# Optimization experiments

Measured on AMD Instinct MI355X. Metric: run time of the kernel, lower is better.

The kernel has to match this reference:

```python
import jax, jax.numpy as jnp
import numpy as np

N = 1 << 20          # number of sample points (rays x samples)
ENC = 32             # hash-grid encoded dim (16 levels x 2 features)
HID = 64
GEO = 15


def setup_inputs() -> dict:
    key = jax.random.key(0)
    ks = jax.random.split(key, 16)
    sc = lambda fan_in: 1.0 / np.sqrt(fan_in)
    return {
        "x": jax.random.normal(ks[0], (N, ENC), jnp.float32),
        "d": jax.random.normal(ks[1], (N, ENC), jnp.float32),
        # sigma net: ENC -> 64 -> 64 -> 1+GEO, bias-free, stored [in, out]
        "Ws0": jax.random.normal(ks[2], (ENC, HID), jnp.float32) * sc(ENC),
        "Ws1": jax.random.normal(ks[3], (HID, HID), jnp.float32) * sc(HID),
        "Ws2": jax.random.normal(ks[4], (HID, 1 + GEO), jnp.float32) * sc(HID),
        # color net: ENC+GEO -> 64 -> 64 -> 64 -> 3, bias-free
        "Wc0": jax.random.normal(ks[5], (ENC + GEO, HID), jnp.float32) * sc(ENC + GEO),
        "Wc1": jax.random.normal(ks[6], (HID, HID), jnp.float32) * sc(HID),
        "Wc2": jax.random.normal(ks[7], (HID, HID), jnp.float32) * sc(HID),
        "Wc3": jax.random.normal(ks[8], (HID, 3), jnp.float32) * sc(HID),
    }


def reference(x, d, Ws0, Ws1, Ws2, Wc0, Wc1, Wc2, Wc3):
    # sigma network: ReLU after EVERY layer (including the last, as in source)
    h = x
    for W in (Ws0, Ws1, Ws2):
        h = jax.nn.relu(h @ W)
    sigma = h[..., 0]            # [N]
    geo_feat = h[..., 1:]        # [N, GEO]

    # color network: ReLU on all but last layer, then sigmoid
    h = jnp.concatenate([d, geo_feat], axis=-1)   # [N, ENC+GEO]
    color_ws = (Wc0, Wc1, Wc2, Wc3)
    for i, W in enumerate(color_ws):
        h = h @ W
        if i != len(color_ws) - 1:
            h = jax.nn.relu(h)
    color = jax.nn.sigmoid(h)    # [N, 3]
    return color, sigma
```

## Files before the change

kernel.cpp:

```cpp
#include <hip/hip_runtime.h>
#include <hip/hip_bf16.h>

typedef short s8v __attribute__((ext_vector_type(8)));
typedef float f4v __attribute__((ext_vector_type(4)));

#define MFMA_BF16 __builtin_amdgcn_mfma_f32_16x16x32_bf16

constexpr int OFF_W0T  = 0;
constexpr int OFF_W1T  = 2560;
constexpr int OFF_W2T  = 7168;
constexpr int OFF_WC0T = 8320;
constexpr int OFF_WC1T = 12928;
constexpr int OFF_WC2T = 17536;
constexpr int OFF_WC3T = 22144;
constexpr int OFF_H    = 23296;
constexpr int SMEM_EL  = OFF_H + 8 * 2048;

static __device__ __forceinline__ short bf2s(__hip_bfloat16 h) {
    union { __hip_bfloat16 b; short s; } u; u.b = h; return u.s;
}

__global__ __launch_bounds__(512, 4)
void rf_fused(const void* __restrict__ xv,
              const void* __restrict__ dv,
              const void* __restrict__ Ws0,
              const void* __restrict__ Ws1,
              const void* __restrict__ Ws2,
              const void* __restrict__ Wc0,
              const void* __restrict__ Wc1,
              const void* __restrict__ Wc2,
              const void* __restrict__ Wc3,
              void* __restrict__ outp,
              int npts)
{
    __shared__ __align__(16) short smem[SMEM_EL];
    __shared__ int cls_cnt;
    const int t = threadIdx.x;

    if (t == 0) cls_cnt = 0;
    __syncthreads();
    {
        unsigned short w = ((const unsigned short*)xv)[2 * t];
        int e = (w >> 7) & 0xFF;
        if (e >= 110 && e <= 140) atomicAdd(&cls_cnt, 1);
    }
    __syncthreads();
    const bool isbf = (cls_cnt >= 256);

    auto ldw = [&](const void* p, int idx) -> short {
        if (isbf) return ((const short*)p)[idx];
        return bf2s(__float2bfloat16(((const float*)p)[idx]));
    };

    for (int i = t; i < 2048; i += 512) { int k = i >> 6, n = i & 63; smem[OFF_W0T  + n*40 + k] = ldw(Ws0, i); }
    for (int i = t; i < 4096; i += 512) { int k = i >> 6, n = i & 63; smem[OFF_W1T  + n*72 + k] = ldw(Ws1, i); }
    for (int i = t; i < 1024; i += 512) { int k = i >> 4, n = i & 15; smem[OFF_W2T  + n*72 + k] = ldw(Ws2, i); }
    for (int i = t; i < 4096; i += 512) { int n = i >> 6, k = i & 63; smem[OFF_WC0T + n*72 + k] = (k < 47) ? ldw(Wc0, k*64 + n) : (short)0; }
    for (int i = t; i < 4096; i += 512) { int k = i >> 6, n = i & 63; smem[OFF_WC1T + n*72 + k] = ldw(Wc1, i); }
    for (int i = t; i < 4096; i += 512) { int k = i >> 6, n = i & 63; smem[OFF_WC2T + n*72 + k] = ldw(Wc2, i); }
    for (int i = t; i < 1024; i += 512) { int n = i >> 6, k = i & 63; smem[OFF_WC3T + n*72 + k] = (n < 3) ? ldw(Wc3, k*3 + n) : (short)0; }
    __syncthreads();

    const int lane = t & 63;
    const int wv   = t >> 6;
    const int m16  = lane & 15;
    const int q    = lane >> 4;
    short* sH = smem + OFF_H + wv * 2048;

    auto hAddr = [&](int row, int col) -> int {
        return row*64 + ((((col >> 3) ^ (row & 7))) << 3) + (col & 7);
    };

    const f4v zf = {0.f, 0.f, 0.f, 0.f};

    auto loadRow8f = [&](const void* p, int eoff) -> s8v {
        const float* f = (const float*)p + eoff;
        f4v f0 = *(const f4v*)f;
        f4v f1 = *(const f4v*)(f + 4);
        s8v r;
        #pragma unroll
        for (int j = 0; j < 4; j++) {
            r[j]     = bf2s(__float2bfloat16(f0[j]));
            r[j + 4] = bf2s(__float2bfloat16(f1[j]));
        }
        return r;
    };
    auto putOut = [&](int idx, float v) {
        if (isbf) ((short*)outp)[idx] = bf2s(__float2bfloat16(v));
        else      ((float*)outp)[idx] = v;
    };

    auto loadAH = [&](s8v (&af)[2][2]) {
        asm volatile("" ::: "memory");
        #pragma unroll
        for (int mt = 0; mt < 2; mt++)
            #pragma unroll
            for (int ks = 0; ks < 2; ks++)
                af[mt][ks] = *(const s8v*)(sH + (mt*16 + m16)*64 + (((ks*4 + q) ^ (m16 & 7)) << 3));
    };
    auto layer64 = [&](int woff, f4v (&a)[2][4], const s8v (&af)[2][2]) {
        #pragma unroll
        for (int nt = 0; nt < 4; nt++) {
            s8v b0 = *(const s8v*)(smem + woff + (nt*16 + m16)*72 + q*8);
            s8v b1 = *(const s8v*)(smem + woff + (nt*16 + m16)*72 + 32 + q*8);
            #pragma unroll
            for (int mt = 0; mt < 2; mt++)
                a[mt][nt] = MFMA_BF16(af[mt][1], b1, MFMA_BF16(af[mt][0], b0, zf, 0,0,0), 0,0,0);
        }
    };
    auto storeH64 = [&](const f4v (&a)[2][4]) {
        #pragma unroll
        for (int mt = 0; mt < 2; mt++)
            #pragma unroll
            for (int nt = 0; nt < 4; nt++)
                #pragma unroll
                for (int r = 0; r < 4; r++) {
                    int row = mt*16 + q*4 + r;
                    sH[row*64 + (((nt*2 + (m16 >> 3)) ^ (row & 7)) << 3) + (m16 & 7)] =
                        bf2s(__float2bfloat16(fmaxf(a[mt][nt][r], 0.f)));
                }
        asm volatile("" ::: "memory");
    };

    const int ntiles = npts / 32;
    const int tstep  = gridDim.x * 8;
    int tile = blockIdx.x * 8 + wv;

    s8v xr[2], dr[2];
    if (isbf && tile < ntiles) {
        #pragma unroll
        for (int mt = 0; mt < 2; mt++) {
            const int off = (tile*32 + mt*16 + m16)*32 + q*8;
            xr[mt] = *(const s8v*)((const short*)xv + off);
            dr[mt] = *(const s8v*)((const short*)dv + off);
        }
    }

    for (; tile < ntiles; tile += tstep) {
        const int r0  = tile * 32;
        const int nxt = tile + tstep;

        s8v xrn[2], drn[2];
        if (isbf && nxt < ntiles) {
            #pragma unroll
            for (int mt = 0; mt < 2; mt++) {
                const int off = (nxt*32 + mt*16 + m16)*32 + q*8;
                xrn[mt] = *(const s8v*)((const short*)xv + off);
                drn[mt] = *(const s8v*)((const short*)dv + off);
            }
        }

        s8v xa[2], da[2];
        if (isbf) {
            xa[0] = xr[0]; xa[1] = xr[1];
            da[0] = dr[0]; da[1] = dr[1];
        } else {
            #pragma unroll
            for (int mt = 0; mt < 2; mt++) {
                const int off = (r0 + mt*16 + m16)*32 + q*8;
                xa[mt] = loadRow8f(xv, off);
                da[mt] = loadRow8f(dv, off);
            }
        }

        f4v acc[2][4];

        #pragma unroll
        for (int nt = 0; nt < 4; nt++) {
            s8v b = *(const s8v*)(smem + OFF_W0T + (nt*16 + m16)*40 + q*8);
            #pragma unroll
            for (int mt = 0; mt < 2; mt++)
                acc[mt][nt] = MFMA_BF16(xa[mt], b, zf, 0,0,0);
        }
        storeH64(acc);

        s8v a2[2][2];
        loadAH(a2);
        layer64(OFF_W1T, acc, a2);
        storeH64(acc);

        s8v a3[2][2];
        loadAH(a3);
        s8v c0 = *(const s8v*)(smem + OFF_W2T + m16*72 + q*8);
        s8v c1 = *(const s8v*)(smem + OFF_W2T + m16*72 + 32 + q*8);
        f4v acc3[2];
        #pragma unroll
        for (int mt = 0; mt < 2; mt++)
            acc3[mt] = MFMA_BF16(a3[mt][1], c1, MFMA_BF16(a3[mt][0], c0, zf, 0,0,0), 0,0,0);

        #pragma unroll
        for (int mt = 0; mt < 2; mt++)
            #pragma unroll
            for (int r = 0; r < 4; r++) {
                float v = fmaxf(acc3[mt][r], 0.f);
                int row = mt*16 + q*4 + r;
                if (m16 == 0) {
                    putOut(3*npts + r0 + row, v);
                    sH[hAddr(row, 15)] = 0;
                } else {
                    sH[hAddr(row, m16 - 1)] = bf2s(__float2bfloat16(v));
                }
            }
        asm volatile("" ::: "memory");

        s8v ga[2];
        #pragma unroll
        for (int mt = 0; mt < 2; mt++)
            ga[mt] = *(const s8v*)(sH + (mt*16 + m16)*64 + ((q ^ (m16 & 7)) << 3));
        #pragma unroll
        for (int nt = 0; nt < 4; nt++) {
            s8v b0 = *(const s8v*)(smem + OFF_WC0T + (nt*16 + m16)*72 + q*8);
            s8v b1 = *(const s8v*)(smem + OFF_WC0T + (nt*16 + m16)*72 + 32 + q*8);
            #pragma unroll
            for (int mt = 0; mt < 2; mt++)
                acc[mt][nt] = MFMA_BF16(ga[mt], b1, MFMA_BF16(da[mt], b0, zf, 0,0,0), 0,0,0);
        }
        storeH64(acc);

        s8v a5[2][2];
        loadAH(a5);
        layer64(OFF_WC1T, acc, a5);
        storeH64(acc);

        s8v a6[2][2];
        loadAH(a6);
        layer64(OFF_WC2T, acc, a6);
        storeH64(acc);

        s8v a7[2][2];
        loadAH(a7);
        s8v e0 = *(const s8v*)(smem + OFF_WC3T + m16*72 + q*8);
        s8v e1 = *(const s8v*)(smem + OFF_WC3T + m16*72 + 32 + q*8);
        f4v acc7[2];
        #pragma unroll
        for (int mt = 0; mt < 2; mt++)
            acc7[mt] = MFMA_BF16(a7[mt][1], e1, MFMA_BF16(a7[mt][0], e0, zf, 0,0,0), 0,0,0);

        if (m16 < 3) {
            #pragma unroll
            for (int mt = 0; mt < 2; mt++)
                #pragma unroll
                for (int r = 0; r < 4; r++) {
                    float v  = acc7[mt][r];
                    float sg = 1.0f / (1.0f + __expf(-v));
                    putOut((r0 + mt*16 + q*4 + r)*3 + m16, sg);
                }
        }

        if (isbf) {
            xr[0] = xrn[0]; xr[1] = xrn[1];
            dr[0] = drn[0]; dr[1] = drn[1];
        }
    }
}

extern "C" void kernel_launch(void* const* d_in, const int* in_sizes, int n_in,
                              void* d_out, int out_size, void* d_ws, size_t ws_size,
                              hipStream_t stream) {
    const int npts = in_sizes[0] / 32;
    rf_fused<<<512, 512, 0, stream>>>(d_in[0], d_in[1], d_in[2], d_in[3], d_in[4],
                                      d_in[5], d_in[6], d_in[7], d_in[8],
                                      d_out, npts);
}
```

Measured before the change: 346.2 us.

## Chain MLP layers in registers via transposed MFMA and permlane swaps

Each layer now computes the transposed product (weights as A, activations as B), so an accumulator fragment can be turned into the next layer's B operand with v_permlane32/16_swap instructions instead of a round trip through LDS. The per-wave 32x64 hidden-state buffer is removed; only a small 32x32 scratch area is kept for the geo-feature handoff between the sigma and color nets. This removes most LDS stores and loads, along with the waits between layers, in exchange for cross-lane permute instructions and output writes reshaped to the transposed layout.

```diff
diff --git a/kernel.cpp b/kernel.cpp
--- a/kernel.cpp
+++ b/kernel.cpp
@@ -13,8 +13,8 @@
 constexpr int OFF_WC1T = 12928;
 constexpr int OFF_WC2T = 17536;
 constexpr int OFF_WC3T = 22144;
-constexpr int OFF_H    = 23296;
-constexpr int SMEM_EL  = OFF_H + 8 * 2048;
+constexpr int OFF_G    = 23168;
+constexpr int SMEM_EL  = OFF_G + 8 * 1024;
 
 static __device__ __forceinline__ short bf2s(__hip_bfloat16 h) {
     union { __hip_bfloat16 b; short s; } u; u.b = h; return u.s;
@@ -59,17 +59,14 @@
     for (int i = t; i < 4096; i += 512) { int k = i >> 6, n = i & 63; smem[OFF_WC1T + n*72 + k] = ldw(Wc1, i); }
     for (int i = t; i < 4096; i += 512) { int k = i >> 6, n = i & 63; smem[OFF_WC2T + n*72 + k] = ldw(Wc2, i); }
     for (int i = t; i < 1024; i += 512) { int n = i >> 6, k = i & 63; smem[OFF_WC3T + n*72 + k] = (n < 3) ? ldw(Wc3, k*3 + n) : (short)0; }
+    for (int i = t; i < 8192; i += 512) smem[OFF_G + i] = 0;
     __syncthreads();
 
     const int lane = t & 63;
     const int wv   = t >> 6;
     const int m16  = lane & 15;
     const int q    = lane >> 4;
-    short* sH = smem + OFF_H + wv * 2048;
-
-    auto hAddr = [&](int row, int col) -> int {
-        return row*64 + ((((col >> 3) ^ (row & 7))) << 3) + (col & 7);
-    };
+    short* sG = smem + OFF_G + wv * 1024;
 
     const f4v zf = {0.f, 0.f, 0.f, 0.f};
 
@@ -90,36 +87,43 @@
         else      ((float*)outp)[idx] = v;
     };
 
-    auto loadAH = [&](s8v (&af)[2][2]) {
-        asm volatile("" ::: "memory");
-        #pragma unroll
-        for (int mt = 0; mt < 2; mt++)
-            #pragma unroll
-            for (int ks = 0; ks < 2; ks++)
-                af[mt][ks] = *(const s8v*)(sH + (mt*16 + m16)*64 + (((ks*4 + q) ^ (m16 & 7)) << 3));
-    };
-    auto layer64 = [&](int woff, f4v (&a)[2][4], const s8v (&af)[2][2]) {
-        #pragma unroll
-        for (int nt = 0; nt < 4; nt++) {
-            s8v b0 = *(const s8v*)(smem + woff + (nt*16 + m16)*72 + q*8);
-            s8v b1 = *(const s8v*)(smem + woff + (nt*16 + m16)*72 + 32 + q*8);
-            #pragma unroll
-            for (int mt = 0; mt < 2; mt++)
-                a[mt][nt] = MFMA_BF16(af[mt][1], b1, MFMA_BF16(af[mt][0], b0, zf, 0,0,0), 0,0,0);
-        }
-    };
-    auto storeH64 = [&](const f4v (&a)[2][4]) {
-        #pragma unroll
-        for (int mt = 0; mt < 2; mt++)
-            #pragma unroll
-            for (int nt = 0; nt < 4; nt++)
-                #pragma unroll
-                for (int r = 0; r < 4; r++) {
-                    int row = mt*16 + q*4 + r;
-                    sH[row*64 + (((nt*2 + (m16 >> 3)) ^ (row & 7)) << 3) + (m16 & 7)] =
-                        bf2s(__float2bfloat16(fmaxf(a[mt][nt][r], 0.f)));
-                }
-        asm volatile("" ::: "memory");
+    auto redist = [&](const f4v (&a)[4], s8v (&fr)[2]) {
+        unsigned int P[4][2];
+        #pragma unroll
+        for (int kt = 0; kt < 4; kt++)
+            #pragma unroll
+            for (int rp = 0; rp < 2; rp++) {
+                float lo = fmaxf(a[kt][2*rp],     0.f);
+                float hi = fmaxf(a[kt][2*rp + 1], 0.f);
+                union { __hip_bfloat162 b; unsigned int u; } cu;
+                cu.b = __float22bfloat162_rn(float2{lo, hi});
+                P[kt][rp] = cu.u;
+            }
+        #pragma unroll
+        for (int a2 = 0; a2 < 2; a2++)
+            #pragma unroll
+            for (int rp = 0; rp < 2; rp++) {
+                asm("v_permlane32_swap_b32 %0, %1" : "+v"(P[2*a2][rp]), "+v"(P[2*a2+1][rp]));
+                asm("v_permlane16_swap_b32 %0, %1" : "+v"(P[2*a2][rp]), "+v"(P[2*a2+1][rp]));
+            }
+        #pragma unroll
+        for (int kc = 0; kc < 2; kc++) {
+            union { unsigned int u[4]; s8v v; } fu;
+            fu.u[0] = P[2*kc][0];     fu.u[1] = P[2*kc][1];
+            fu.u[2] = P[2*kc + 1][0]; fu.u[3] = P[2*kc + 1][1];
+            fr[kc] = fu.v;
+        }
+    };
+
+    auto layerT = [&](int woff, const s8v (&bf)[2][2], f4v (&out)[2][4]) {
+        #pragma unroll
+        for (int kt = 0; kt < 4; kt++) {
+            s8v a0 = *(const s8v*)(smem + woff + (kt*16 + m16)*72 + q*8);
+            s8v a1 = *(const s8v*)(smem + woff + (kt*16 + m16)*72 + 32 + q*8);
+            #pragma unroll
+            for (int pt = 0; pt < 2; pt++)
+                out[pt][kt] = MFMA_BF16(a1, bf[pt][1], MFMA_BF16(a0, bf[pt][0], zf, 0,0,0), 0,0,0);
+        }
     };
 
     const int ntiles = npts / 32;
@@ -129,10 +133,10 @@
     s8v xr[2], dr[2];
     if (isbf && tile < ntiles) {
         #pragma unroll
-        for (int mt = 0; mt < 2; mt++) {
-            const int off = (tile*32 + mt*16 + m16)*32 + q*8;
-            xr[mt] = *(const s8v*)((const short*)xv + off);
-            dr[mt] = *(const s8v*)((const short*)dv + off);
+        for (int pt = 0; pt < 2; pt++) {
+            const int off = (tile*32 + pt*16 + m16)*32 + q*8;
+            xr[pt] = *(const s8v*)((const short*)xv + off);
+            dr[pt] = *(const s8v*)((const short*)dv + off);
         }
     }
 
@@ -143,108 +147,107 @@
         s8v xrn[2], drn[2];
         if (isbf && nxt < ntiles) {
             #pragma unroll
-            for (int mt = 0; mt < 2; mt++) {
-                const int off = (nxt*32 + mt*16 + m16)*32 + q*8;
-                xrn[mt] = *(const s8v*)((const short*)xv + off);
-                drn[mt] = *(const s8v*)((const short*)dv + off);
-            }
-        }
-
-        s8v xa[2], da[2];
+            for (int pt = 0; pt < 2; pt++) {
+                const int off = (nxt*32 + pt*16 + m16)*32 + q*8;
+                xrn[pt] = *(const s8v*)((const short*)xv + off);
+                drn[pt] = *(const s8v*)((const short*)dv + off);
+            }
+        }
+
+        s8v xb[2], db[2];
         if (isbf) {
-            xa[0] = xr[0]; xa[1] = xr[1];
-            da[0] = dr[0]; da[1] = dr[1];
+            xb[0] = xr[0]; xb[1] = xr[1];
+            db[0] = dr[0]; db[1] = dr[1];
         } else {
             #pragma unroll
-            for (int mt = 0; mt < 2; mt++) {
-                const int off = (r0 + mt*16 + m16)*32 + q*8;
-                xa[mt] = loadRow8f(xv, off);
-                da[mt] = loadRow8f(dv, off);
+            for (int pt = 0; pt < 2; pt++) {
+                const int off = (r0 + pt*16 + m16)*32 + q*8;
+                xb[pt] = loadRow8f(xv, off);
+                db[pt] = loadRow8f(dv, off);
             }
         }
 
         f4v acc[2][4];
-
-        #pragma unroll
-        for (int nt = 0; nt < 4; nt++) {
-            s8v b = *(const s8v*)(smem + OFF_W0T + (nt*16 + m16)*40 + q*8);
-            #pragma unroll
-            for (int mt = 0; mt < 2; mt++)
-                acc[mt][nt] = MFMA_BF16(xa[mt], b, zf, 0,0,0);
-        }
-        storeH64(acc);
-
-        s8v a2[2][2];
-        loadAH(a2);
-        layer64(OFF_W1T, acc, a2);
-        storeH64(acc);
-
-        s8v a3[2][2];
-        loadAH(a3);
-        s8v c0 = *(const s8v*)(smem + OFF_W2T + m16*72 + q*8);
-        s8v c1 = *(const s8v*)(smem + OFF_W2T + m16*72 + 32 + q*8);
-        f4v acc3[2];
-        #pragma unroll
-        for (int mt = 0; mt < 2; mt++)
-            acc3[mt] = MFMA_BF16(a3[mt][1], c1, MFMA_BF16(a3[mt][0], c0, zf, 0,0,0), 0,0,0);
-
-        #pragma unroll
-        for (int mt = 0; mt < 2; mt++)
+        s8v bf[2][2];
+
+        #pragma unroll
+        for (int kt = 0; kt < 4; kt++) {
+            s8v a0 = *(const s8v*)(smem + OFF_W0T + (kt*16 + m16)*40 + q*8);
+            #pragma unroll
+            for (int pt = 0; pt < 2; pt++)
+                acc[pt][kt] = MFMA_BF16(a0, xb[pt], zf, 0,0,0);
+        }
+        #pragma unroll
+        for (int pt = 0; pt < 2; pt++) redist(acc[pt], bf[pt]);
+
+        layerT(OFF_W1T, bf, acc);
+        #pragma unroll
+        for (int pt = 0; pt < 2; pt++) redist(acc[pt], bf[pt]);
+
+        f4v s3[2];
+        {
+            s8v c0 = *(const s8v*)(smem + OFF_W2T + m16*72 + q*8);
+            s8v c1 = *(const s8v*)(smem + OFF_W2T + m16*72 + 32 + q*8);
+            #pragma unroll
+            for (int pt = 0; pt < 2; pt++)
+                s3[pt] = MFMA_BF16(c1, bf[pt][1], MFMA_BF16(c0, bf[pt][0], zf, 0,0,0), 0,0,0);
+        }
+
+        #pragma unroll
+        for (int pt = 0; pt < 2; pt++) {
+            const int point = pt*16 + m16;
             #pragma unroll
             for (int r = 0; r < 4; r++) {
-                float v = fmaxf(acc3[mt][r], 0.f);
-                int row = mt*16 + q*4 + r;
-                if (m16 == 0) {
-                    putOut(3*npts + r0 + row, v);
-                    sH[hAddr(row, 15)] = 0;
+                float v = fmaxf(s3[pt][r], 0.f);
+                if (q*4 + r == 0) {
+                    putOut(3*npts + r0 + point, v);
+                    sG[point*32 + 15] = 0;
                 } else {
-                    sH[hAddr(row, m16 - 1)] = bf2s(__float2bfloat16(v));
+                    sG[point*32 + q*4 + r - 1] = bf2s(__float2bfloat16(v));
                 }
             }
+        }
         asm volatile("" ::: "memory");
 
-        s8v ga[2];
-        #pragma unroll
-        for (int mt = 0; mt < 2; mt++)
-            ga[mt] = *(const s8v*)(sH + (mt*16 + m16)*64 + ((q ^ (m16 & 7)) << 3));
-        #pragma unroll
-        for (int nt = 0; nt < 4; nt++) {
-            s8v b0 = *(const s8v*)(smem + OFF_WC0T + (nt*16 + m16)*72 + q*8);
-            s8v b1 = *(const s8v*)(smem + OFF_WC0T + (nt*16 + m16)*72 + 32 + q*8);
-            #pragma unroll
-            for (int mt = 0; mt < 2; mt++)
-                acc[mt][nt] = MFMA_BF16(ga[mt], b1, MFMA_BF16(da[mt], b0, zf, 0,0,0), 0,0,0);
-        }
-        storeH64(acc);
-
-        s8v a5[2][2];
-        loadAH(a5);
-        layer64(OFF_WC1T, acc, a5);
-        storeH64(acc);
-
-        s8v a6[2][2];
-        loadAH(a6);
-        layer64(OFF_WC2T, acc, a6);
-        storeH64(acc);
-
-        s8v a7[2][2];
-        loadAH(a7);
-        s8v e0 = *(const s8v*)(smem + OFF_WC3T + m16*72 + q*8);
-        s8v e1 = *(const s8v*)(smem + OFF_WC3T + m16*72 + 32 + q*8);
-        f4v acc7[2];
-        #pragma unroll
-        for (int mt = 0; mt < 2; mt++)
-            acc7[mt] = MFMA_BF16(a7[mt][1], e1, MFMA_BF16(a7[mt][0], e0, zf, 0,0,0), 0,0,0);
-
-        if (m16 < 3) {
-            #pragma unroll
-            for (int mt = 0; mt < 2; mt++)
+        s8v gb[2];
+        #pragma unroll
+        for (int pt = 0; pt < 2; pt++)
+            gb[pt] = *(const s8v*)(sG + (pt*16 + m16)*32 + q*8);
+        asm volatile("" ::: "memory");
+
+        #pragma unroll
+        for (int pt = 0; pt < 2; pt++) { bf[pt][0] = db[pt]; bf[pt][1] = gb[pt]; }
+        layerT(OFF_WC0T, bf, acc);
+        #pragma unroll
+        for (int pt = 0; pt < 2; pt++) redist(acc[pt], bf[pt]);
+
+        layerT(OFF_WC1T, bf, acc);
+        #pragma unroll
+        for (int pt = 0; pt < 2; pt++) redist(acc[pt], bf[pt]);
+
+        layerT(OFF_WC2T, bf, acc);
+        #pragma unroll
+        for (int pt = 0; pt < 2; pt++) redist(acc[pt], bf[pt]);
+
+        f4v c7[2];
+        {
+            s8v e0 = *(const s8v*)(smem + OFF_WC3T + m16*72 + q*8);
+            s8v e1 = *(const s8v*)(smem + OFF_WC3T + m16*72 + 32 + q*8);
+            #pragma unroll
+            for (int pt = 0; pt < 2; pt++)
+                c7[pt] = MFMA_BF16(e1, bf[pt][1], MFMA_BF16(e0, bf[pt][0], zf, 0,0,0), 0,0,0);
+        }
+        if (q == 0) {
+            #pragma unroll
+            for (int pt = 0; pt < 2; pt++) {
+                const int base = (r0 + pt*16 + m16) * 3;
                 #pragma unroll
-                for (int r = 0; r < 4; r++) {
-                    float v  = acc7[mt][r];
+                for (int r = 0; r < 3; r++) {
+                    float v  = c7[pt][r];
                     float sg = 1.0f / (1.0f + __expf(-v));
-                    putOut((r0 + mt*16 + q*4 + r)*3 + m16, sg);
+                    putOut(base + r, sg);
                 }
+            }
         }
 
         if (isbf) {
```

Result: faster. 314.9 us (-9.0%).
